# Performance work log

Measured on AMD Instinct MI355X. Metric: run time of the kernel, lower is better.

The kernel has to match this reference:

```python
import jax, jax.numpy as jnp
import numpy as np

B, T, C, H, MAX_LEN = 16, 512, 1024, 16, 512
D = C // H  # head_dim = 64

def setup_inputs() -> dict:
    key = jax.random.key(0)
    ks = jax.random.split(key, 10)
    s = 1.0 / np.sqrt(C)
    return {
        "x": jax.random.normal(ks[0], (B, T, C), dtype=jnp.float32),
        "Wq": jax.random.normal(ks[1], (C, C), dtype=jnp.float32) * s,
        "bq": jnp.zeros((C,), dtype=jnp.float32),
        "Wk": jax.random.normal(ks[2], (C, C), dtype=jnp.float32) * s,
        "bk": jnp.zeros((C,), dtype=jnp.float32),
        "Wv": jax.random.normal(ks[3], (C, C), dtype=jnp.float32) * s,
        "bv": jnp.zeros((C,), dtype=jnp.float32),
        "Wo": jax.random.normal(ks[4], (C, C), dtype=jnp.float32) * s,
        "bo": jnp.zeros((C,), dtype=jnp.float32),
        "rel_pos_bias": jax.random.normal(ks[5], (H, MAX_LEN, MAX_LEN), dtype=jnp.float32) * 0.02,
    }

def reference(x, Wq, bq, Wk, bk, Wv, bv, Wo, bo, rel_pos_bias):
    scale = 1.0 / jnp.sqrt(jnp.float32(D))
    # projections (torch Linear: x @ W.T + b), reshape to (B,H,T,D)
    def proj(W, b):
        return (x @ W.T + b).reshape(B, T, H, D).transpose(0, 2, 1, 3)
    q, k, v = proj(Wq, bq), proj(Wk, bk), proj(Wv, bv)
    attn = jnp.einsum('bhtd,bhsd->bhts', q, k) * scale  # (B,H,T,T)
    attn = attn + rel_pos_bias[None, :, :T, :T]
    causal = jnp.triu(jnp.ones((T, T), dtype=bool), k=1)
    attn = jnp.where(causal[None, None], -jnp.inf, attn)
    attn = jax.nn.softmax(attn, axis=-1)  # dropout p=0 (eval) -> identity
    out = jnp.einsum('bhts,bhsd->bhtd', attn, v)
    out = out.transpose(0, 2, 1, 3).reshape(B, T, C)
    return out @ Wo.T + bo
```

## Files before the change

### kernel.cpp

```cpp
#include <hip/hip_runtime.h>
#include <stdint.h>
#include <math.h>

#define DEV static __device__ __forceinline__

typedef __attribute__((ext_vector_type(8))) __bf16 bf16x8;
typedef __attribute__((ext_vector_type(4))) float f32x4;
typedef unsigned short u16;

DEV u16 f2b(float f) {
  union { float f; uint32_t u; } x; x.f = f;
  uint32_t r = x.u + 0x7fffu + ((x.u >> 16) & 1u);
  return (u16)(r >> 16);
}

DEV uint32_t pk2(float a, float b) {
  return (uint32_t)f2b(a) | ((uint32_t)f2b(b) << 16);
}

DEV float b2f_lo(uint32_t u) { return __uint_as_float(u << 16); }
DEV float b2f_hi(uint32_t u) { return __uint_as_float(u & 0xffff0000u); }

DEV void glds16(const void* g, void* l) {
  __builtin_amdgcn_global_load_lds(
      (const __attribute__((address_space(1))) void*)g,
      (__attribute__((address_space(3))) void*)l, 16, 0, 0);
}

DEV f32x4 mfma16(bf16x8 a, bf16x8 b, f32x4 c) {
  return __builtin_amdgcn_mfma_f32_16x16x32_bf16(a, b, c, 0, 0, 0);
}

#define BAR() __builtin_amdgcn_s_barrier()
#define WAIT_LGKM()                                      \
  {                                                      \
    asm volatile("s_waitcnt lgkmcnt(0)" ::: "memory");   \
    __builtin_amdgcn_sched_barrier(0);                   \
  }
#define WAIT_VM4() asm volatile("s_waitcnt vmcnt(4)" ::: "memory")
#define WAIT_VM0() asm volatile("s_waitcnt vmcnt(0)" ::: "memory")

__global__ __launch_bounds__(256) void cvt_all(
    const float* __restrict__ x, const float* __restrict__ Wq,
    const float* __restrict__ Wk, const float* __restrict__ Wv,
    const float* __restrict__ Wo, const float* __restrict__ bias,
    u16* __restrict__ xb, u16* __restrict__ wqkv, u16* __restrict__ wo,
    u16* __restrict__ biasb) {
  size_t i = ((size_t)blockIdx.x * 256 + threadIdx.x) * 4;
  const float* s;
  u16* d;
  size_t off;
  float scale = 1.0f;
  if (i < 8388608)        { s = x;  d = xb;             off = i; }
  else if (i < 9437184)   { s = Wq; d = wqkv;           off = i - 8388608; }
  else if (i < 10485760)  { s = Wk; d = wqkv + 1048576; off = i - 9437184; }
  else if (i < 11534336)  { s = Wv; d = wqkv + 2097152; off = i - 10485760; }
  else if (i < 12582912)  { s = Wo; d = wo;             off = i - 11534336; }
  else { s = bias; d = biasb; off = i - 12582912; scale = 1.44269504f; }
  float4 v = *(const float4*)(s + off);
  ushort4 o;
  o.x = f2b(v.x * scale); o.y = f2b(v.y * scale);
  o.z = f2b(v.z * scale); o.w = f2b(v.w * scale);
  *(ushort4*)(d + off) = o;
}


DEV void stage_slot(const u16* A, const u16* Bw, int m0, int n0, int col,
                    int wave, int srow, int scol, u16* slotA, u16* slotB) {
#pragma unroll
  for (int cc = 0; cc < 2; ++cc) {
    int unit = wave * 2 + cc;
    int r = unit * 16 + srow;
    glds16(A + (size_t)(m0 + r) * 1024 + col + scol, slotA + unit * 512);
    glds16(Bw + (size_t)(n0 + r) * 1024 + col + scol, slotB + unit * 512);
  }
}

DEV void load_frags(const u16* Rbase, const u16* Cbase, int wr, int wc,
                    int c16, int swz, bf16x8 rf[4], bf16x8 cf[4]) {
#pragma unroll
  for (int i = 0; i < 4; ++i)
    rf[i] = *(const bf16x8*)&Rbase[(wr * 64 + i * 16 + c16) * 32 + swz];
#pragma unroll
  for (int i = 0; i < 4; ++i)
    cf[i] = *(const bf16x8*)&Cbase[(wc * 64 + i * 16 + c16) * 32 + swz];
}

DEV void mfma_all(bf16x8 rf[4], bf16x8 cf[4], f32x4 acc[4][4]) {
#pragma unroll
  for (int i = 0; i < 4; ++i)
#pragma unroll
    for (int j = 0; j < 4; ++j) acc[i][j] = mfma16(rf[i], cf[j], acc[i][j]);
}

DEV void gemm_core(const u16* A, const u16* Bw, int m0, int n0, bool vblk,
                   int wave, int lane, u16 (*lsA)[4096], u16 (*lsB)[4096],
                   f32x4 acc[4][4]) {
  int q16 = lane >> 4, c16 = lane & 15;
  int wm = wave >> 1, wn = wave & 1;
  int wr = vblk ? wn : wm, wc = vblk ? wm : wn;
  int srow = lane >> 2;
  int scol = ((lane & 3) ^ ((lane >> 3) & 3)) * 8;
  int swz = (q16 ^ ((c16 >> 1) & 3)) * 8;

  stage_slot(A, Bw, m0, n0, 0, wave, srow, scol, lsA[0], lsB[0]);
  stage_slot(A, Bw, m0, n0, 32, wave, srow, scol, lsA[1], lsB[1]);
  WAIT_VM4();
  BAR();

#pragma unroll
  for (int g = 0; g < 32; ++g) {
    const int slot = g % 3;
    const u16* Rb = vblk ? &lsB[slot][0] : &lsA[slot][0];
    const u16* Cb = vblk ? &lsA[slot][0] : &lsB[slot][0];
    bf16x8 rf[4], cf[4];
    load_frags(Rb, Cb, wr, wc, c16, swz, rf, cf);
    if (g < 30)
      stage_slot(A, Bw, m0, n0, (g + 2) * 32, wave, srow, scol,
                 lsA[(g + 2) % 3], lsB[(g + 2) % 3]);
    BAR();
    WAIT_LGKM();
    __builtin_amdgcn_s_setprio(1);
    mfma_all(rf, cf, acc);
    __builtin_amdgcn_s_setprio(0);
    if (g < 30) { WAIT_VM4(); } else if (g == 30) { WAIT_VM0(); }
    BAR();
  }
}

__global__ __launch_bounds__(256, 3) void gemm_qkv(
    const u16* __restrict__ A, const u16* __restrict__ Bw,
    const float* __restrict__ bq, const float* __restrict__ bk,
    const float* __restrict__ bv,
    u16* __restrict__ qo, u16* __restrict__ ko, u16* __restrict__ vto) {
  __shared__ u16 lsA[3][4096];
  __shared__ u16 lsB[3][4096];
  int tid = threadIdx.x, wave = tid >> 6, lane = tid & 63;
  int q16 = lane >> 4, c16 = lane & 15;
  int m0 = blockIdx.y * 128, n0 = blockIdx.x * 128;
  int wm = wave >> 1, wn = wave & 1;
  const bool vblk = (n0 >= 2048);

  f32x4 acc[4][4];
#pragma unroll
  for (int i = 0; i < 4; ++i)
#pragma unroll
    for (int j = 0; j < 4; ++j) acc[i][j] = (f32x4)0.0f;

  gemm_core(A, Bw, m0, n0, vblk, wave, lane, lsA, lsB, acc);

  if (!vblk) {
#pragma unroll
    for (int mt = 0; mt < 4; ++mt) {
#pragma unroll
      for (int nt = 0; nt < 4; ++nt) {
        int n = n0 + wn * 64 + nt * 16 + c16;
        int which = n >> 10;
        int nl = n & 1023;
        int hh = nl >> 6, d = nl & 63;
        float bias = (which == 0 ? bq : bk)[nl];
        u16* dst = (which == 0 ? qo : ko);
#pragma unroll
        for (int r = 0; r < 4; ++r) {
          int m = m0 + wm * 64 + mt * 16 + q16 * 4 + r;
          int b = m >> 9, t = m & 511;
          size_t bh = (size_t)b * 16 + hh;
          dst[(bh * 512 + t) * 72 + d] = f2b(acc[mt][nt][r] + bias);
        }
      }
    }
  } else {
#pragma unroll
    for (int it = 0; it < 4; ++it) {
      int nbase = n0 + wn * 64 + it * 16 + q16 * 4;
      float4 bvv = *(const float4*)(bv + (nbase & 1023));
#pragma unroll
      for (int jt = 0; jt < 4; ++jt) {
        int m = m0 + wm * 64 + jt * 16 + c16;
        int b = m >> 9, t = m & 511;
        size_t bh4 = ((size_t)b * 16) * 4;
#pragma unroll
        for (int r = 0; r < 4; ++r) {
          int nl = (nbase + r) & 1023;
          int hh = nl >> 6, d = nl & 63;
          float bias = ((const float*)&bvv)[r];
          vto[((bh4 + (size_t)hh * 4 + (t >> 7)) * 64 + d) * 136 + (t & 127)] =
              f2b(acc[it][jt][r] + bias);
        }
      }
    }
  }
}

__global__ __launch_bounds__(256, 3) void attn_kernel(
    const u16* __restrict__ qglob, const u16* __restrict__ kglob,
    const u16* __restrict__ vtglob, const u16* __restrict__ biasb,
    u16* __restrict__ og) {
  __shared__ u16 lsK[128 * 72];
  __shared__ u16 lsV[64 * 136];
  __shared__ u16 lsP[4 * 32 * 68];

  int tid = threadIdx.x, wave = tid >> 6, lane = tid & 63;
  int q16 = lane >> 4, c16 = lane & 15;
  u16* lsPw = lsP + wave * (32 * 68);

  int p = blockIdx.x;
  int bx, bh, bx2 = -1, bh2 = 0;
  if (p < 256)      { bx = 3; bh = p; }
  else if (p < 512) { bx = 2; bh = p - 256; bx2 = 0; bh2 = p - 256; }
  else              { int q = p - 512; bx = 1; bh = 2 * q; bx2 = 1; bh2 = 2 * q + 1; }

  for (;;) {
    int b = bh >> 4, h = bh & 15;
    int q0 = bx * 128;

    const u16* qbase = qglob + (size_t)bh * (512 * 72) + (size_t)q0 * 72;
    const u16* kbase = kglob + (size_t)bh * (512 * 72);
    const u16* vbase = vtglob + (size_t)bh * 4 * (64 * 136);

    for (int i = wave; i < 18; i += 4)
      glds16(qbase + (size_t)i * 512 + lane * 8, lsK + i * 512);
    __syncthreads();
    bf16x8 qf[2][2];
#pragma unroll
    for (int nt = 0; nt < 2; ++nt)
#pragma unroll
      for (int ks = 0; ks < 2; ++ks)
        qf[nt][ks] = *(const bf16x8*)&lsK[(wave * 32 + nt * 16 + c16) * 72 +
                                          ks * 32 + q16 * 8];

    f32x4 oacc[2][4];
#pragma unroll
    for (int i = 0; i < 2; ++i)
#pragma unroll
      for (int j = 0; j < 4; ++j) oacc[i][j] = (f32x4)0.0f;
    float mold[2] = {-INFINITY, -INFINITY};
    float lsum[2] = {0.0f, 0.0f};
    const float SCL = 0.18033688f;

    for (int st = 0; st <= bx; ++st) {
      bool diag = (st == bx);
      __syncthreads();
      const u16* kt = kbase + (size_t)st * (128 * 72);
      for (int i = wave; i < 18; i += 4)
        glds16(kt + (size_t)i * 512 + lane * 8, lsK + i * 512);
      const u16* vt = vbase + (size_t)st * (64 * 136);
      for (int i = wave; i < 17; i += 4)
        glds16(vt + (size_t)i * 512 + lane * 8, lsV + i * 512);

      uint2 ub[2][8];
#pragma unroll
      for (int nt = 0; nt < 2; ++nt) {
        int qgl = q0 + wave * 32 + nt * 16 + c16;
        const u16* bp =
            biasb + ((size_t)h * 512 + qgl) * 512 + st * 128 + q16 * 4;
#pragma unroll
        for (int mt = 0; mt < 8; ++mt) ub[nt][mt] = *(const uint2*)(bp + mt * 16);
      }
      __syncthreads();

      f32x4 sa[8][2];
#pragma unroll
      for (int mt = 0; mt < 8; ++mt) {
        sa[mt][0] = (f32x4)0.0f;
        sa[mt][1] = (f32x4)0.0f;
      }
      int mtmax = diag ? 2 * wave + 2 : 8;
#pragma unroll
      for (int mt = 0; mt < 8; ++mt) {
        if (mt < mtmax) {
#pragma unroll
          for (int ks = 0; ks < 2; ++ks) {
            bf16x8 kf =
                *(const bf16x8*)&lsK[(mt * 16 + c16) * 72 + ks * 32 + q16 * 8];
            sa[mt][0] = mfma16(kf, qf[0][ks], sa[mt][0]);
            sa[mt][1] = mfma16(kf, qf[1][ks], sa[mt][1]);
          }
        }
      }

      float alpha[2];
#pragma unroll
      for (int nt = 0; nt < 2; ++nt) {
#pragma unroll
        for (int mt = 0; mt < 8; ++mt) {
          uint32_t lo = ub[nt][mt].x, hi = ub[nt][mt].y;
          f32x4 bv;
          bv[0] = b2f_lo(lo); bv[1] = b2f_hi(lo);
          bv[2] = b2f_lo(hi); bv[3] = b2f_hi(hi);
          sa[mt][nt] = sa[mt][nt] * SCL + bv;
        }
        if (diag) {
#pragma unroll
          for (int mt = 0; mt < 8; ++mt) {
            int d0 = mt * 16 + q16 * 4 - wave * 32 - nt * 16 - c16;
#pragma unroll
            for (int r = 0; r < 4; ++r)
              if (d0 + r > 0) sa[mt][nt][r] = -INFINITY;
          }
        }
        f32x4 m4 = sa[0][nt];
#pragma unroll
        for (int mt = 1; mt < 8; ++mt) {
          f32x4 v = sa[mt][nt];
          m4[0] = fmaxf(m4[0], v[0]); m4[1] = fmaxf(m4[1], v[1]);
          m4[2] = fmaxf(m4[2], v[2]); m4[3] = fmaxf(m4[3], v[3]);
        }
        float mx = fmaxf(fmaxf(m4[0], m4[1]), fmaxf(m4[2], m4[3]));
        mx = fmaxf(mx, __shfl_xor(mx, 16));
        mx = fmaxf(mx, __shfl_xor(mx, 32));
        float mnew = fmaxf(mold[nt], mx);
        alpha[nt] = exp2f(mold[nt] - mnew);
        mold[nt] = mnew;
        f32x4 s4 = (f32x4)0.0f;
#pragma unroll
        for (int mt = 0; mt < 8; ++mt) {
          f32x4 pq;
          pq[0] = exp2f(sa[mt][nt][0] - mnew);
          pq[1] = exp2f(sa[mt][nt][1] - mnew);
          pq[2] = exp2f(sa[mt][nt][2] - mnew);
          pq[3] = exp2f(sa[mt][nt][3] - mnew);
          sa[mt][nt] = pq;
          s4 += pq;
        }
        float ss = (s4[0] + s4[1]) + (s4[2] + s4[3]);
        ss += __shfl_xor(ss, 16);
        ss += __shfl_xor(ss, 32);
        lsum[nt] = lsum[nt] * alpha[nt] + ss;
      }

#pragma unroll
      for (int mo = 0; mo < 2; ++mo) {
        f32x4 av;
#pragma unroll
        for (int r = 0; r < 4; ++r) av[r] = __shfl(alpha[mo], q16 * 4 + r);
#pragma unroll
        for (int dt = 0; dt < 4; ++dt) oacc[mo][dt] *= av;
      }

      int G = diag ? wave + 1 : 4;
#pragma unroll
      for (int hf = 0; hf < 2; ++hf) {
        if (hf * 2 < G) {
#pragma unroll
          for (int nt = 0; nt < 2; ++nt)
#pragma unroll
            for (int mt4 = 0; mt4 < 4; ++mt4) {
              f32x4 pv = sa[hf * 4 + mt4][nt];
              uint2 w;
              w.x = pk2(pv[0], pv[1]);
              w.y = pk2(pv[2], pv[3]);
              *(uint2*)&lsPw[(nt * 16 + c16) * 68 + mt4 * 16 + q16 * 4] = w;
            }
#pragma unroll
          for (int ksh = 0; ksh < 2; ++ksh) {
            if (hf * 2 + ksh < G) {
              bf16x8 pf0 =
                  *(const bf16x8*)&lsPw[c16 * 68 + ksh * 32 + q16 * 8];
              bf16x8 pf1 =
                  *(const bf16x8*)&lsPw[(16 + c16) * 68 + ksh * 32 + q16 * 8];
#pragma unroll
              for (int dt = 0; dt < 4; ++dt) {
                bf16x8 vf = *(const bf16x8*)&lsV[(dt * 16 + c16) * 136 +
                                                 hf * 64 + ksh * 32 + q16 * 8];
                oacc[0][dt] = mfma16(pf0, vf, oacc[0][dt]);
                oacc[1][dt] = mfma16(pf1, vf, oacc[1][dt]);
              }
            }
          }
        }
      }
    }

#pragma unroll
    for (int mo = 0; mo < 2; ++mo) {
      f32x4 lv;
#pragma unroll
      for (int r = 0; r < 4; ++r) lv[r] = __shfl(lsum[mo], q16 * 4 + r);
#pragma unroll
      for (int r = 0; r < 4; ++r) {
        int tg = q0 + wave * 32 + mo * 16 + q16 * 4 + r;
        float inv = 1.0f / lv[r];
#pragma unroll
        for (int dt = 0; dt < 4; ++dt)
          og[((size_t)b * 512 + tg) * 1024 + h * 64 + dt * 16 + c16] =
              f2b(oacc[mo][dt][r] * inv);
      }
    }

    if (bx2 < 0) break;
    __syncthreads();
    bx = bx2; bh = bh2; bx2 = -1;
  }
}

__global__ __launch_bounds__(256, 3) void gemm_out(
    const u16* __restrict__ A, const u16* __restrict__ W,
    const float* __restrict__ bo, float* __restrict__ out) {
  __shared__ u16 lsA[3][4096];
  __shared__ u16 lsB[3][4096];
  int tid = threadIdx.x, wave = tid >> 6, lane = tid & 63;
  int q16 = lane >> 4, c16 = lane & 15;
  int m0 = blockIdx.y * 128, n0 = blockIdx.x * 128;
  int wm = wave >> 1, wn = wave & 1;

  f32x4 acc[4][4];
#pragma unroll
  for (int i = 0; i < 4; ++i)
#pragma unroll
    for (int j = 0; j < 4; ++j) acc[i][j] = (f32x4)0.0f;

  gemm_core(A, W, m0, n0, false, wave, lane, lsA, lsB, acc);

#pragma unroll
  for (int mt = 0; mt < 4; ++mt) {
#pragma unroll
    for (int nt = 0; nt < 4; ++nt) {
      int n = n0 + wn * 64 + nt * 16 + c16;
      float bias = bo[n];
#pragma unroll
      for (int r = 0; r < 4; ++r) {
        int m = m0 + wm * 64 + mt * 16 + q16 * 4 + r;
        out[(size_t)m * 1024 + n] = acc[mt][nt][r] + bias;
      }
    }
  }
}

extern "C" void kernel_launch(void* const* d_in, const int* in_sizes, int n_in,
                              void* d_out, int out_size, void* d_ws, size_t ws_size,
                              hipStream_t stream) {
  const float* x    = (const float*)d_in[0];
  const float* Wq   = (const float*)d_in[1];
  const float* bq   = (const float*)d_in[2];
  const float* Wk   = (const float*)d_in[3];
  const float* bk   = (const float*)d_in[4];
  const float* Wv   = (const float*)d_in[5];
  const float* bv   = (const float*)d_in[6];
  const float* Wo   = (const float*)d_in[7];
  const float* bo   = (const float*)d_in[8];
  const float* bias = (const float*)d_in[9];
  float* out = (float*)d_out;

  const size_t MB = 1u << 20;
  char* ws = (char*)d_ws;
  u16* xb    = (u16*)(ws);
  u16* wqkv  = (u16*)(ws + 16 * MB);
  u16* wo    = (u16*)(ws + 22 * MB);
  u16* biasb = (u16*)(ws + 24 * MB);
  u16* qb    = (u16*)(ws + 32 * MB);
  u16* kb    = (u16*)(ws + 50 * MB);
  u16* vtb   = (u16*)(ws + 68 * MB);
  u16* ab    = xb;

  cvt_all<<<16384, 256, 0, stream>>>(x, Wq, Wk, Wv, Wo, bias,
                                     xb, wqkv, wo, biasb);
  gemm_qkv<<<dim3(24, 64), 256, 0, stream>>>(xb, wqkv, bq, bk, bv, qb, kb, vtb);
  attn_kernel<<<dim3(640), 256, 0, stream>>>(qb, kb, vtb, biasb, ab);
  gemm_out<<<dim3(8, 64), 256, 0, stream>>>(ab, wo, bo, out);
}
```

Measured before the change: 265.0 us.

## Enlarge QKV GEMM tile to 256x128 with eight waves per block

The QKV projection GEMM now runs 512 threads per block on a 256-row by 128-column tile. The A tile doubles in LDS and each wave issues three async global-to-LDS loads per stage, so the vmcnt wait drops to 3. This halves the number of M blocks and reuses each staged weight tile across twice as many rows, which cuts global and L2 traffic for the weights. The output GEMM keeps the old 128x128 path as a separate core. In exchange, LDS per block rises to 72 KB, and the launch bounds of (512,4) may cap registers tightly enough to cause spills or lower occupancy.

```diff
diff --git a/kernel.cpp b/kernel.cpp
--- a/kernel.cpp
+++ b/kernel.cpp
@@ -37,6 +37,7 @@
     asm volatile("s_waitcnt lgkmcnt(0)" ::: "memory");   \
     __builtin_amdgcn_sched_barrier(0);                   \
   }
+#define WAIT_VM3() asm volatile("s_waitcnt vmcnt(3)" ::: "memory")
 #define WAIT_VM4() asm volatile("s_waitcnt vmcnt(4)" ::: "memory")
 #define WAIT_VM0() asm volatile("s_waitcnt vmcnt(0)" ::: "memory")
 
@@ -65,15 +66,13 @@
 }
 
 
-DEV void stage_slot(const u16* A, const u16* Bw, int m0, int n0, int col,
-                    int wave, int srow, int scol, u16* slotA, u16* slotB) {
-#pragma unroll
-  for (int cc = 0; cc < 2; ++cc) {
-    int unit = wave * 2 + cc;
-    int r = unit * 16 + srow;
-    glds16(A + (size_t)(m0 + r) * 1024 + col + scol, slotA + unit * 512);
-    glds16(Bw + (size_t)(n0 + r) * 1024 + col + scol, slotB + unit * 512);
-  }
+DEV void stage_slot8(const u16* A, const u16* Bw, int m0, int n0, int col,
+                     int wave, int srow, int scol, u16* slotA, u16* slotB) {
+  const u16* srcA = A + (size_t)(m0 + wave * 32 + srow) * 1024 + col + scol;
+  glds16(srcA, slotA + wave * 1024);
+  glds16(srcA + (size_t)16 * 1024, slotA + wave * 1024 + 512);
+  glds16(Bw + (size_t)(n0 + wave * 16 + srow) * 1024 + col + scol,
+         slotB + wave * 512);
 }
 
 DEV void load_frags(const u16* Rbase, const u16* Cbase, int wr, int wc,
@@ -93,9 +92,9 @@
     for (int j = 0; j < 4; ++j) acc[i][j] = mfma16(rf[i], cf[j], acc[i][j]);
 }
 
-DEV void gemm_core(const u16* A, const u16* Bw, int m0, int n0, bool vblk,
-                   int wave, int lane, u16 (*lsA)[4096], u16 (*lsB)[4096],
-                   f32x4 acc[4][4]) {
+DEV void gemm_core8(const u16* A, const u16* Bw, int m0, int n0, bool vblk,
+                    int wave, int lane, u16 (*lsA)[8192], u16 (*lsB)[4096],
+                    f32x4 acc[4][4]) {
   int q16 = lane >> 4, c16 = lane & 15;
   int wm = wave >> 1, wn = wave & 1;
   int wr = vblk ? wn : wm, wc = vblk ? wm : wn;
@@ -103,9 +102,9 @@
   int scol = ((lane & 3) ^ ((lane >> 3) & 3)) * 8;
   int swz = (q16 ^ ((c16 >> 1) & 3)) * 8;
 
-  stage_slot(A, Bw, m0, n0, 0, wave, srow, scol, lsA[0], lsB[0]);
-  stage_slot(A, Bw, m0, n0, 32, wave, srow, scol, lsA[1], lsB[1]);
-  WAIT_VM4();
+  stage_slot8(A, Bw, m0, n0, 0, wave, srow, scol, lsA[0], lsB[0]);
+  stage_slot8(A, Bw, m0, n0, 32, wave, srow, scol, lsA[1], lsB[1]);
+  WAIT_VM3();
   BAR();
 
 #pragma unroll
@@ -116,8 +115,52 @@
     bf16x8 rf[4], cf[4];
     load_frags(Rb, Cb, wr, wc, c16, swz, rf, cf);
     if (g < 30)
-      stage_slot(A, Bw, m0, n0, (g + 2) * 32, wave, srow, scol,
-                 lsA[(g + 2) % 3], lsB[(g + 2) % 3]);
+      stage_slot8(A, Bw, m0, n0, (g + 2) * 32, wave, srow, scol,
+                  lsA[(g + 2) % 3], lsB[(g + 2) % 3]);
+    BAR();
+    WAIT_LGKM();
+    __builtin_amdgcn_s_setprio(1);
+    mfma_all(rf, cf, acc);
+    __builtin_amdgcn_s_setprio(0);
+    if (g < 30) { WAIT_VM3(); } else if (g == 30) { WAIT_VM0(); }
+    BAR();
+  }
+}
+
+
+DEV void stage_slot4(const u16* A, const u16* Bw, int m0, int n0, int col,
+                     int wave, int srow, int scol, u16* slotA, u16* slotB) {
+#pragma unroll
+  for (int cc = 0; cc < 2; ++cc) {
+    int unit = wave * 2 + cc;
+    int r = unit * 16 + srow;
+    glds16(A + (size_t)(m0 + r) * 1024 + col + scol, slotA + unit * 512);
+    glds16(Bw + (size_t)(n0 + r) * 1024 + col + scol, slotB + unit * 512);
+  }
+}
+
+DEV void gemm_core4(const u16* A, const u16* Bw, int m0, int n0,
+                    int wave, int lane, u16 (*lsA)[4096], u16 (*lsB)[4096],
+                    f32x4 acc[4][4]) {
+  int q16 = lane >> 4, c16 = lane & 15;
+  int wm = wave >> 1, wn = wave & 1;
+  int srow = lane >> 2;
+  int scol = ((lane & 3) ^ ((lane >> 3) & 3)) * 8;
+  int swz = (q16 ^ ((c16 >> 1) & 3)) * 8;
+
+  stage_slot4(A, Bw, m0, n0, 0, wave, srow, scol, lsA[0], lsB[0]);
+  stage_slot4(A, Bw, m0, n0, 32, wave, srow, scol, lsA[1], lsB[1]);
+  WAIT_VM4();
+  BAR();
+
+#pragma unroll
+  for (int g = 0; g < 32; ++g) {
+    const int slot = g % 3;
+    bf16x8 rf[4], cf[4];
+    load_frags(&lsA[slot][0], &lsB[slot][0], wm, wn, c16, swz, rf, cf);
+    if (g < 30)
+      stage_slot4(A, Bw, m0, n0, (g + 2) * 32, wave, srow, scol,
+                  lsA[(g + 2) % 3], lsB[(g + 2) % 3]);
     BAR();
     WAIT_LGKM();
     __builtin_amdgcn_s_setprio(1);
@@ -128,16 +171,16 @@
   }
 }
 
-__global__ __launch_bounds__(256, 3) void gemm_qkv(
+__global__ __launch_bounds__(512, 4) void gemm_qkv(
     const u16* __restrict__ A, const u16* __restrict__ Bw,
     const float* __restrict__ bq, const float* __restrict__ bk,
     const float* __restrict__ bv,
     u16* __restrict__ qo, u16* __restrict__ ko, u16* __restrict__ vto) {
-  __shared__ u16 lsA[3][4096];
+  __shared__ u16 lsA[3][8192];
   __shared__ u16 lsB[3][4096];
   int tid = threadIdx.x, wave = tid >> 6, lane = tid & 63;
   int q16 = lane >> 4, c16 = lane & 15;
-  int m0 = blockIdx.y * 128, n0 = blockIdx.x * 128;
+  int m0 = blockIdx.y * 256, n0 = blockIdx.x * 128;
   int wm = wave >> 1, wn = wave & 1;
   const bool vblk = (n0 >= 2048);
 
@@ -147,7 +190,7 @@
 #pragma unroll
     for (int j = 0; j < 4; ++j) acc[i][j] = (f32x4)0.0f;
 
-  gemm_core(A, Bw, m0, n0, vblk, wave, lane, lsA, lsB, acc);
+  gemm_core8(A, Bw, m0, n0, vblk, wave, lane, lsA, lsB, acc);
 
   if (!vblk) {
 #pragma unroll
@@ -410,7 +453,7 @@
 #pragma unroll
     for (int j = 0; j < 4; ++j) acc[i][j] = (f32x4)0.0f;
 
-  gemm_core(A, W, m0, n0, false, wave, lane, lsA, lsB, acc);
+  gemm_core4(A, W, m0, n0, wave, lane, lsA, lsB, acc);
 
 #pragma unroll
   for (int mt = 0; mt < 4; ++mt) {
@@ -455,7 +498,7 @@
 
   cvt_all<<<16384, 256, 0, stream>>>(x, Wq, Wk, Wv, Wo, bias,
                                      xb, wqkv, wo, biasb);
-  gemm_qkv<<<dim3(24, 64), 256, 0, stream>>>(xb, wqkv, bq, bk, bv, qb, kb, vtb);
+  gemm_qkv<<<dim3(24, 32), 512, 0, stream>>>(xb, wqkv, bq, bk, bv, qb, kb, vtb);
   attn_kernel<<<dim3(640), 256, 0, stream>>>(qb, kb, vtb, biasb, ab);
   gemm_out<<<dim3(8, 64), 256, 0, stream>>>(ab, wo, bo, out);
 }
```

New measurement: 262.4 us. About the same (-1.0%).
